# Kernel optimization log

Hardware: AMD Instinct MI355X
Metric: run time of the kernel (lower is better)

The kernel has to match this reference:

```python
import jax, jax.numpy as jnp
import numpy as np

NUM_HEADS = 16


def setup_inputs() -> dict:
    key = jax.random.key(0)
    k1, k2, k3, k4 = jax.random.split(key, 4)
    B, N, C = 4, 1024, 1024
    x = jax.random.normal(k1, (B, N, C), dtype=jnp.float32)
    mask = jnp.ones((B, N), dtype=jnp.float32)  # 1 = visible token
    # 0.02 init scale keeps logits in a sane range (avoids saturated softmax)
    W_qkv = jax.random.normal(k2, (C, 3 * C), dtype=jnp.float32) * 0.02
    W_proj = jax.random.normal(k3, (C, C), dtype=jnp.float32) * 0.02
    b_proj = jax.random.normal(k4, (C,), dtype=jnp.float32) * 0.02
    return {"x": x, "mask": mask, "W_qkv": W_qkv, "W_proj": W_proj, "b_proj": b_proj}


def reference(x, mask, W_qkv, W_proj, b_proj):
    B, N, C = x.shape
    H = NUM_HEADS
    D = C // H
    scale = D ** -0.5
    qkv = (x @ W_qkv).reshape(B, N, 3, H, D)
    q, k, v = qkv[:, :, 0], qkv[:, :, 1], qkv[:, :, 2]  # each [B, N, H, D]
    attn = jnp.einsum("bnhd,bmhd->bhnm", q, k) * scale  # [B, H, N, N]
    attn = attn + (1.0 - mask)[:, None, None, :] * -5.0  # additive mask penalty
    attn = jax.nn.softmax(attn, axis=-1)
    out = jnp.einsum("bhnm,bmhd->bnhd", attn, v).reshape(B, N, C)
    return out @ W_proj + b_proj
```

## Files before the change

kernel.cpp:

```cpp
#include <hip/hip_runtime.h>

typedef __attribute__((ext_vector_type(8))) short bf16x8;
typedef __attribute__((ext_vector_type(4))) float f32x4;
typedef __attribute__((ext_vector_type(16))) float f32x16;
typedef __attribute__((ext_vector_type(4))) float fl4;
typedef __attribute__((ext_vector_type(8))) unsigned short u16x8;
typedef __attribute__((ext_vector_type(4))) unsigned short u16x4;
typedef __attribute__((ext_vector_type(2))) int i32x2;
typedef __attribute__((ext_vector_type(4))) int i32x4;

#define MFMA16(A,B,C) __builtin_amdgcn_mfma_f32_16x16x32_bf16((A),(B),(C),0,0,0)
#define MFMA32(A,B,C) __builtin_amdgcn_mfma_f32_32x32x16_bf16((A),(B),(C),0,0,0)

__device__ __forceinline__ unsigned short f2bf_bits(float x) {
  union { float f; unsigned u; } v; v.f = x;
  unsigned r = v.u + 0x7fffu + ((v.u >> 16) & 1u);
  return (unsigned short)(r >> 16);
}

__device__ __forceinline__ void gload_lds16(const void* g, void* l) {
  __builtin_amdgcn_global_load_lds((const __attribute__((address_space(1))) void*)g,
                                   (__attribute__((address_space(3))) void*)l, 16, 0, 0);
}

__device__ __forceinline__ bf16x8 lds_frag(const char* base, int row, int bir) {
  int off = (row << 7) + bir;
  off ^= (row & 7) << 4;
  return *(const bf16x8*)(base + off);
}

__device__ __forceinline__ int cvtpk_bf16(float a, float b) {
  int r; asm("v_cvt_pk_bf16_f32 %0, %1, %2" : "=v"(r) : "v"(a), "v"(b)); return r;
}

__device__ __forceinline__ void plswap(int& a, int& b) {
#if __has_builtin(__builtin_amdgcn_permlane32_swap)
  i32x2 r = __builtin_amdgcn_permlane32_swap(a, b, false, false);
  a = r[0]; b = r[1];
#else
  asm volatile("s_nop 1\n\tv_permlane32_swap_b32 %0, %1" : "+v"(a), "+v"(b));
#endif
}

__global__ __launch_bounds__(256) void k_cvt(const float* __restrict__ src,
                                             unsigned short* __restrict__ dst, int n) {
  int i = (blockIdx.x * 256 + threadIdx.x) * 8;
  if (i >= n) return;
  fl4 a = *(const fl4*)(src + i);
  fl4 b = *(const fl4*)(src + i + 4);
  u16x8 o;
  o[0] = f2bf_bits(a[0]); o[1] = f2bf_bits(a[1]); o[2] = f2bf_bits(a[2]); o[3] = f2bf_bits(a[3]);
  o[4] = f2bf_bits(b[0]); o[5] = f2bf_bits(b[1]); o[6] = f2bf_bits(b[2]); o[7] = f2bf_bits(b[3]);
  *(u16x8*)(dst + i) = o;
}

__global__ __launch_bounds__(256) void k_tcvt(const float* __restrict__ src,
                                              unsigned short* __restrict__ dst, int NCOL) {
  __shared__ float tile[64][65];
  const int kt = blockIdx.y * 64, nt = blockIdx.x * 64;
  const int t = threadIdx.x;
  {
    int r = t >> 2, c0 = (t & 3) * 16;
    const float* s = src + (size_t)(kt + r) * NCOL + nt + c0;
    #pragma unroll
    for (int j = 0; j < 4; ++j) {
      fl4 v = *(const fl4*)(s + j * 4);
      tile[r][c0 + j * 4 + 0] = v[0]; tile[r][c0 + j * 4 + 1] = v[1];
      tile[r][c0 + j * 4 + 2] = v[2]; tile[r][c0 + j * 4 + 3] = v[3];
    }
  }
  __syncthreads();
  {
    int n = t >> 2, kc = (t & 3) * 16;
    unsigned short* d = dst + (size_t)(nt + n) * 1024 + kt + kc;
    u16x8 o0, o1;
    #pragma unroll
    for (int j = 0; j < 8; ++j) o0[j] = f2bf_bits(tile[kc + j][n]);
    #pragma unroll
    for (int j = 0; j < 8; ++j) o1[j] = f2bf_bits(tile[kc + 8 + j][n]);
    *(u16x8*)d = o0;
    *(u16x8*)(d + 8) = o1;
  }
}

template <int MODE>
__global__ __launch_bounds__(256) void k_gemm(const unsigned short* __restrict__ A,
                                              const unsigned short* __restrict__ Bt,
                                              unsigned short* __restrict__ qp,
                                              unsigned short* __restrict__ kp,
                                              unsigned short* __restrict__ vtp,
                                              const float* __restrict__ bias,
                                              float* __restrict__ outp) {
  __shared__ char lA[16384], lB[16384];
  const int tid = threadIdx.x, lane = tid & 63, w = tid >> 6;
  const int wm = w >> 1, wn = w & 1;
  const int m0 = blockIdx.y * 128, n0 = blockIdx.x * 128;
  const char* Ab = (const char*)A + (size_t)m0 * 2048;
  const char* Bb = (const char*)Bt + (size_t)n0 * 2048;

  f32x4 acc[4][4];
  #pragma unroll
  for (int mi = 0; mi < 4; ++mi)
    #pragma unroll
    for (int ni = 0; ni < 4; ++ni) acc[mi][ni] = f32x4{0.f, 0.f, 0.f, 0.f};

  for (int kt = 0; kt < 16; ++kt) {
    #pragma unroll
    for (int i = 0; i < 4; ++i) {
      int c = i * 256 + tid;
      int row = c >> 3, cc = c & 7, ccs = cc ^ (row & 7);
      char* dstA = lA + (i * 256 + w * 64) * 16;
      char* dstB = lB + (i * 256 + w * 64) * 16;
      gload_lds16(Ab + (size_t)row * 2048 + kt * 128 + ccs * 16, dstA);
      gload_lds16(Bb + (size_t)row * 2048 + kt * 128 + ccs * 16, dstB);
    }
    __syncthreads();
    #pragma unroll
    for (int ks = 0; ks < 2; ++ks) {
      bf16x8 af[4], bfv[4];
      #pragma unroll
      for (int mi = 0; mi < 4; ++mi)
        af[mi] = lds_frag(lA, wm * 64 + mi * 16 + (lane & 15), ks * 64 + ((lane >> 4) << 4));
      #pragma unroll
      for (int ni = 0; ni < 4; ++ni)
        bfv[ni] = lds_frag(lB, wn * 64 + ni * 16 + (lane & 15), ks * 64 + ((lane >> 4) << 4));
      #pragma unroll
      for (int mi = 0; mi < 4; ++mi)
        #pragma unroll
        for (int ni = 0; ni < 4; ++ni)
          acc[mi][ni] = MFMA16(af[mi], bfv[ni], acc[mi][ni]);
    }
    __syncthreads();
  }

  if (MODE == 0) {
    #pragma unroll
    for (int mi = 0; mi < 4; ++mi) {
      int row0 = m0 + wm * 64 + mi * 16 + ((lane >> 4) << 2);
      int bb = row0 >> 10, nn0 = row0 & 1023;
      #pragma unroll
      for (int ni = 0; ni < 4; ++ni) {
        int col = n0 + wn * 64 + ni * 16 + (lane & 15);
        int tt = col >> 10, rem = col & 1023, h = rem >> 6, d = rem & 63;
        f32x4 a = acc[mi][ni];
        if (tt == 2) {
          u16x4 pv;
          pv[0] = f2bf_bits(a[0]); pv[1] = f2bf_bits(a[1]);
          pv[2] = f2bf_bits(a[2]); pv[3] = f2bf_bits(a[3]);
          *(u16x4*)(vtp + (((size_t)(bb * 16 + h) * 64 + d) << 10) + nn0) = pv;
        } else {
          unsigned short* dst = (tt == 0) ? qp : kp;
          size_t base = ((size_t)(bb * 16 + h)) << 16;
          #pragma unroll
          for (int r = 0; r < 4; ++r)
            dst[base + (size_t)(nn0 + r) * 64 + d] = f2bf_bits(a[r]);
        }
      }
    }
  } else {
    #pragma unroll
    for (int mi = 0; mi < 4; ++mi) {
      int row0 = m0 + wm * 64 + mi * 16 + ((lane >> 4) << 2);
      #pragma unroll
      for (int ni = 0; ni < 4; ++ni) {
        int col = n0 + wn * 64 + ni * 16 + (lane & 15);
        float bv = bias[col];
        f32x4 a = acc[mi][ni];
        #pragma unroll
        for (int r = 0; r < 4; ++r)
          outp[(size_t)(row0 + r) * 1024 + col] = a[r] + bv;
      }
    }
  }
}

__global__ __launch_bounds__(256, 4) void k_attn(const unsigned short* __restrict__ qp,
                                                 const unsigned short* __restrict__ kp,
                                                 const unsigned short* __restrict__ vtp,
                                                 const float* __restrict__ mask,
                                                 unsigned short* __restrict__ aop) {
  __shared__ __align__(16) char lds[32768];
  const int tid = threadIdx.x, lane = tid & 63, w = tid >> 6;
  const int hi = lane >> 5, lq = lane & 31;
  const int pair = w >> 1;
  const int g = blockIdx.x;
  const int bh = (g & 7) * 8 + (g >> 7);
  const int qc = (g >> 3) & 15;
  const int b = bh >> 4, h = bh & 15;
  const char* kb = (const char*)(kp + ((size_t)bh << 16));
  const char* vb = (const char*)(vtp + ((size_t)bh << 16));
  const unsigned short* qh = qp + ((size_t)bh << 16);
  const float* mrow = mask + b * 1024 + pair * 512;
  const int q0 = qc * 64 + (w & 1) * 32;

  const int krow = tid >> 3, kslot = tid & 7;
  const int kcc = kslot ^ (krow & 7);
  const char* gKA = kb + (size_t)krow * 128 + kcc * 16;
  const char* gKB = gKA + 512 * 128;
  const int vrow = tid >> 2, vslot = tid & 3;
  const int vcc = vslot ^ ((vrow >> 1) & 3);
  const char* gVA = vb + (size_t)vrow * 2048 + vcc * 16;
  const char* gVB = gVA + 512 * 2;
  char* const dK = lds + tid * 16;
  char* const dV = lds + 8192 + tid * 16;

  const char* const myK = lds + pair * 4096;
  const char* const myV = lds + 8192 + pair * 4096;
  int kfo[4], vfo[4];
  #pragma unroll
  for (int dc = 0; dc < 4; ++dc)
    kfo[dc] = lq * 128 + (((dc << 1) | hi) ^ (lq & 7)) * 16;
  #pragma unroll
  for (int ks = 0; ks < 2; ++ks)
    #pragma unroll
    for (int nb = 0; nb < 2; ++nb) {
      int row = nb * 32 + lq;
      vfo[ks * 2 + nb] = row * 64 + (((ks << 1) | hi) ^ ((row >> 1) & 3)) * 16;
    }

  bf16x8 qB[4];
  #pragma unroll
  for (int dc = 0; dc < 4; ++dc)
    qB[dc] = *(const bf16x8*)(qh + (q0 + lq) * 64 + dc * 16 + hi * 8);

  i32x4 onesw = {hi == 0 ? 0x3F80 : 0, 0, 0, 0};
  const bf16x8 onesB = __builtin_bit_cast(bf16x8, onesw);

  f32x16 O0, O1;
  #pragma unroll
  for (int i = 0; i < 16; ++i) { O0[i] = 0.f; O1[i] = 0.f; }
  float lsum = 0.f;

#define STAGE(BUF, T)                                                          \
  do {                                                                         \
    gload_lds16(gKA + (T) * 4096, dK + (BUF) * 16384);                         \
    gload_lds16(gKB + (T) * 4096, dK + (BUF) * 16384 + 4096);                  \
    gload_lds16(gVA + (T) * 64,   dV + (BUF) * 16384);                         \
    gload_lds16(gVB + (T) * 64,   dV + (BUF) * 16384 + 4096);                  \
  } while (0)

#define STEP(BUF, T, LAST)                                                     \
  do {                                                                         \
    float mv = mrow[(T) * 32 + lq];                                            \
    if (!(LAST)) STAGE((BUF) ^ 1, (T) + 1);                                    \
    const char* K = myK + (BUF) * 16384;                                       \
    const char* V = myV + (BUF) * 16384;                                       \
    f32x16 acc;                                                                \
    _Pragma("unroll") for (int i = 0; i < 16; ++i) acc[i] = 0.f;               \
    __builtin_amdgcn_s_setprio(1);                                             \
    _Pragma("unroll") for (int dc = 0; dc < 4; ++dc) {                         \
      bf16x8 kf = *(const bf16x8*)(K + kfo[dc]);                               \
      acc = MFMA32(kf, qB[dc], acc);                                           \
    }                                                                          \
    __builtin_amdgcn_s_setprio(0);                                             \
    {                                                                          \
      int bw = (hi == 0) ? (int)f2bf_bits((1.0f - mv) * -40.0f) : 0;           \
      i32x4 bwv = {bw, 0, 0, 0};                                               \
      acc = MFMA32(__builtin_bit_cast(bf16x8, bwv), onesB, acc);               \
    }                                                                          \
    float p[16];                                                               \
    _Pragma("unroll") for (int r = 0; r < 16; ++r) {                           \
      p[r] = exp2f(fmaf(acc[r], 0.18033688f, -5.7707802f));                    \
      lsum += p[r];                                                            \
    }                                                                          \
    int X0 = cvtpk_bf16(p[0], p[1]),   X1 = cvtpk_bf16(p[2], p[3]);            \
    int Y0 = cvtpk_bf16(p[4], p[5]),   Y1 = cvtpk_bf16(p[6], p[7]);            \
    int Z0 = cvtpk_bf16(p[8], p[9]),   Z1 = cvtpk_bf16(p[10], p[11]);          \
    int V0 = cvtpk_bf16(p[12], p[13]), V1 = cvtpk_bf16(p[14], p[15]);          \
    plswap(X0, Y0); plswap(X1, Y1);                                            \
    plswap(Z0, V0); plswap(Z1, V1);                                            \
    i32x4 pa0v = {X0, X1, Y0, Y1};                                             \
    i32x4 pa1v = {Z0, Z1, V0, V1};                                             \
    const bf16x8 PA0 = __builtin_bit_cast(bf16x8, pa0v);                       \
    const bf16x8 PA1 = __builtin_bit_cast(bf16x8, pa1v);                       \
    bf16x8 va0 = *(const bf16x8*)(V + vfo[0]);                                 \
    bf16x8 va1 = *(const bf16x8*)(V + vfo[1]);                                 \
    bf16x8 vb0 = *(const bf16x8*)(V + vfo[2]);                                 \
    bf16x8 vb1 = *(const bf16x8*)(V + vfo[3]);                                 \
    __builtin_amdgcn_s_setprio(1);                                             \
    O0 = MFMA32(PA0, va0, O0);                                                 \
    O1 = MFMA32(PA0, va1, O1);                                                 \
    O0 = MFMA32(PA1, vb0, O0);                                                 \
    O1 = MFMA32(PA1, vb1, O1);                                                 \
    __builtin_amdgcn_s_setprio(0);                                             \
    __syncthreads();                                                           \
  } while (0)

  STAGE(0, 0);
  __syncthreads();
  for (int tt = 0; tt < 8; ++tt) {
    STEP(0, 2 * tt, 0);
    STEP(1, 2 * tt + 1, tt == 7);
  }
#undef STEP
#undef STAGE

  float tot = lsum + __shfl_xor(lsum, 32);
  float* fx = (float*)lds;
  if (pair == 1) {
    int base = (w - 2) * 64 * 34 + lane * 34;
    #pragma unroll
    for (int r = 0; r < 16; ++r) { fx[base + r] = O0[r]; fx[base + 16 + r] = O1[r]; }
    fx[base + 32] = tot;
  }
  __syncthreads();
  if (pair == 0) {
    int base = w * 64 * 34 + lane * 34;
    float invT = 1.0f / (tot + fx[base + 32]);
    #pragma unroll
    for (int r = 0; r < 16; ++r) {
      int qr = (r & 3) + 8 * (r >> 2) + 4 * hi;
      float iv = __shfl(invT, qr);
      float o0 = (O0[r] + fx[base + r]) * iv;
      float o1 = (O1[r] + fx[base + 16 + r]) * iv;
      size_t ob = (size_t)(b * 1024 + q0 + qr) * 1024 + h * 64 + lq;
      aop[ob] = f2bf_bits(o0);
      aop[ob + 32] = f2bf_bits(o1);
    }
  }
}

extern "C" void kernel_launch(void* const* d_in, const int* in_sizes, int n_in,
                              void* d_out, int out_size, void* d_ws, size_t ws_size,
                              hipStream_t stream) {
  const float* x     = (const float*)d_in[0];
  const float* mask  = (const float*)d_in[1];
  const float* wqkv  = (const float*)d_in[2];
  const float* wproj = (const float*)d_in[3];
  const float* bproj = (const float*)d_in[4];
  float* out = (float*)d_out;

  char* ws = (char*)d_ws;
  unsigned short* xb     = (unsigned short*)(ws);
  unsigned short* wqkvt  = (unsigned short*)(ws + 8388608);
  unsigned short* wprojt = (unsigned short*)(ws + 14680064);
  unsigned short* qbuf   = (unsigned short*)(ws + 16777216);
  unsigned short* kbuf   = (unsigned short*)(ws + 25165824);
  unsigned short* vtbuf  = (unsigned short*)(ws + 33554432);
  unsigned short* aobuf  = (unsigned short*)(ws + 41943040);

  k_cvt<<<dim3(2048), dim3(256), 0, stream>>>(x, xb, 4194304);
  k_tcvt<<<dim3(48, 16), dim3(256), 0, stream>>>(wqkv, wqkvt, 3072);
  k_tcvt<<<dim3(16, 16), dim3(256), 0, stream>>>(wproj, wprojt, 1024);
  k_gemm<0><<<dim3(24, 32), dim3(256), 0, stream>>>(xb, wqkvt, qbuf, kbuf, vtbuf, nullptr, nullptr);
  k_attn<<<dim3(1024), dim3(256), 0, stream>>>(qbuf, kbuf, vtbuf, mask, aobuf);
  k_gemm<1><<<dim3(8, 32), dim3(256), 0, stream>>>(aobuf, wprojt, nullptr, nullptr, nullptr, bproj, out);
}
```

Before: 106.3 us.

## Precompute mask bias in convert kernel and fold it into the exp argument

A per-token additive bias (mask penalty combined with the fixed softmax offset, in log2 units) is computed by extra blocks of the conversion kernel. The attention kernel adds this bias inside the exp2 FMA instead of issuing an extra MFMA per tile to inject the mask, and splits the row sum into two accumulators. The two weight-transpose launches are also merged into one to save a launch. This costs vector mask loads per step and a small workspace buffer.

```diff
diff --git a/kernel.cpp b/kernel.cpp
--- a/kernel.cpp
+++ b/kernel.cpp
@@ -43,8 +43,16 @@
 }
 
 __global__ __launch_bounds__(256) void k_cvt(const float* __restrict__ src,
-                                             unsigned short* __restrict__ dst, int n) {
-  int i = (blockIdx.x * 256 + threadIdx.x) * 8;
+                                             unsigned short* __restrict__ dst, int n,
+                                             const float* __restrict__ m,
+                                             float* __restrict__ mb) {
+  int bid = blockIdx.x;
+  if (bid >= 2048) {
+    int i = (bid - 2048) * 256 + threadIdx.x;
+    mb[i] = fmaf(m[i], 7.2134752f, -12.9842554f);
+    return;
+  }
+  int i = (bid * 256 + threadIdx.x) * 8;
   if (i >= n) return;
   fl4 a = *(const fl4*)(src + i);
   fl4 b = *(const fl4*)(src + i + 4);
@@ -54,10 +62,16 @@
   *(u16x8*)(dst + i) = o;
 }
 
-__global__ __launch_bounds__(256) void k_tcvt(const float* __restrict__ src,
-                                              unsigned short* __restrict__ dst, int NCOL) {
+__global__ __launch_bounds__(256) void k_tcvt2(const float* __restrict__ wqkv,
+                                               unsigned short* __restrict__ dqkv,
+                                               const float* __restrict__ wproj,
+                                               unsigned short* __restrict__ dproj) {
   __shared__ float tile[64][65];
-  const int kt = blockIdx.y * 64, nt = blockIdx.x * 64;
+  const int bx = blockIdx.x;
+  const float* src; unsigned short* dst; int NCOL, nt;
+  if (bx < 48) { src = wqkv; dst = dqkv; NCOL = 3072; nt = bx * 64; }
+  else         { src = wproj; dst = dproj; NCOL = 1024; nt = (bx - 48) * 64; }
+  const int kt = blockIdx.y * 64;
   const int t = threadIdx.x;
   {
     int r = t >> 2, c0 = (t & 3) * 16;
@@ -177,7 +191,7 @@
 __global__ __launch_bounds__(256, 4) void k_attn(const unsigned short* __restrict__ qp,
                                                  const unsigned short* __restrict__ kp,
                                                  const unsigned short* __restrict__ vtp,
-                                                 const float* __restrict__ mask,
+                                                 const float* __restrict__ mbias,
                                                  unsigned short* __restrict__ aop) {
   __shared__ __align__(16) char lds[32768];
   const int tid = threadIdx.x, lane = tid & 63, w = tid >> 6;
@@ -190,7 +204,7 @@
   const char* kb = (const char*)(kp + ((size_t)bh << 16));
   const char* vb = (const char*)(vtp + ((size_t)bh << 16));
   const unsigned short* qh = qp + ((size_t)bh << 16);
-  const float* mrow = mask + b * 1024 + pair * 512;
+  const float* mrow = mbias + b * 1024 + pair * 512;
   const int q0 = qc * 64 + (w & 1) * 32;
 
   const int krow = tid >> 3, kslot = tid & 7;
@@ -223,13 +237,10 @@
   for (int dc = 0; dc < 4; ++dc)
     qB[dc] = *(const bf16x8*)(qh + (q0 + lq) * 64 + dc * 16 + hi * 8);
 
-  i32x4 onesw = {hi == 0 ? 0x3F80 : 0, 0, 0, 0};
-  const bf16x8 onesB = __builtin_bit_cast(bf16x8, onesw);
-
   f32x16 O0, O1;
   #pragma unroll
   for (int i = 0; i < 16; ++i) { O0[i] = 0.f; O1[i] = 0.f; }
-  float lsum = 0.f;
+  float lsA = 0.f, lsB = 0.f;
 
 #define STAGE(BUF, T)                                                          \
   do {                                                                         \
@@ -241,7 +252,9 @@
 
 #define STEP(BUF, T, LAST)                                                     \
   do {                                                                         \
-    float mv = mrow[(T) * 32 + lq];                                            \
+    fl4 mw[4];                                                                 \
+    _Pragma("unroll") for (int g4 = 0; g4 < 4; ++g4)                           \
+      mw[g4] = *(const fl4*)(mrow + (T) * 32 + g4 * 8 + hi * 4);               \
     if (!(LAST)) STAGE((BUF) ^ 1, (T) + 1);                                    \
     const char* K = myK + (BUF) * 16384;                                       \
     const char* V = myV + (BUF) * 16384;                                       \
@@ -253,24 +266,19 @@
       acc = MFMA32(kf, qB[dc], acc);                                           \
     }                                                                          \
     __builtin_amdgcn_s_setprio(0);                                             \
-    {                                                                          \
-      int bw = (hi == 0) ? (int)f2bf_bits((1.0f - mv) * -40.0f) : 0;           \
-      i32x4 bwv = {bw, 0, 0, 0};                                               \
-      acc = MFMA32(__builtin_bit_cast(bf16x8, bwv), onesB, acc);               \
-    }                                                                          \
     float p[16];                                                               \
     _Pragma("unroll") for (int r = 0; r < 16; ++r) {                           \
-      p[r] = exp2f(fmaf(acc[r], 0.18033688f, -5.7707802f));                    \
-      lsum += p[r];                                                            \
+      p[r] = exp2f(fmaf(acc[r], 0.18033688f, mw[r >> 2][r & 3]));              \
+      if (r & 1) lsB += p[r]; else lsA += p[r];                                \
     }                                                                          \
     int X0 = cvtpk_bf16(p[0], p[1]),   X1 = cvtpk_bf16(p[2], p[3]);            \
     int Y0 = cvtpk_bf16(p[4], p[5]),   Y1 = cvtpk_bf16(p[6], p[7]);            \
     int Z0 = cvtpk_bf16(p[8], p[9]),   Z1 = cvtpk_bf16(p[10], p[11]);          \
-    int V0 = cvtpk_bf16(p[12], p[13]), V1 = cvtpk_bf16(p[14], p[15]);          \
+    int W0 = cvtpk_bf16(p[12], p[13]), W1 = cvtpk_bf16(p[14], p[15]);          \
     plswap(X0, Y0); plswap(X1, Y1);                                            \
-    plswap(Z0, V0); plswap(Z1, V1);                                            \
+    plswap(Z0, W0); plswap(Z1, W1);                                            \
     i32x4 pa0v = {X0, X1, Y0, Y1};                                             \
-    i32x4 pa1v = {Z0, Z1, V0, V1};                                             \
+    i32x4 pa1v = {Z0, Z1, W0, W1};                                             \
     const bf16x8 PA0 = __builtin_bit_cast(bf16x8, pa0v);                       \
     const bf16x8 PA1 = __builtin_bit_cast(bf16x8, pa1v);                       \
     bf16x8 va0 = *(const bf16x8*)(V + vfo[0]);                                 \
@@ -295,6 +303,7 @@
 #undef STEP
 #undef STAGE
 
+  float lsum = lsA + lsB;
   float tot = lsum + __shfl_xor(lsum, 32);
   float* fx = (float*)lds;
   if (pair == 1) {
@@ -338,11 +347,11 @@
   unsigned short* kbuf   = (unsigned short*)(ws + 25165824);
   unsigned short* vtbuf  = (unsigned short*)(ws + 33554432);
   unsigned short* aobuf  = (unsigned short*)(ws + 41943040);
-
-  k_cvt<<<dim3(2048), dim3(256), 0, stream>>>(x, xb, 4194304);
-  k_tcvt<<<dim3(48, 16), dim3(256), 0, stream>>>(wqkv, wqkvt, 3072);
-  k_tcvt<<<dim3(16, 16), dim3(256), 0, stream>>>(wproj, wprojt, 1024);
+  float*          mbias  = (float*)(ws + 50331648);
+
+  k_cvt<<<dim3(2064), dim3(256), 0, stream>>>(x, xb, 4194304, mask, mbias);
+  k_tcvt2<<<dim3(64, 16), dim3(256), 0, stream>>>(wqkv, wqkvt, wproj, wprojt);
   k_gemm<0><<<dim3(24, 32), dim3(256), 0, stream>>>(xb, wqkvt, qbuf, kbuf, vtbuf, nullptr, nullptr);
-  k_attn<<<dim3(1024), dim3(256), 0, stream>>>(qbuf, kbuf, vtbuf, mask, aobuf);
+  k_attn<<<dim3(1024), dim3(256), 0, stream>>>(qbuf, kbuf, vtbuf, mbias, aobuf);
   k_gemm<1><<<dim3(8, 32), dim3(256), 0, stream>>>(aobuf, wprojt, nullptr, nullptr, nullptr, bproj, out);
 }
```

Result: slower. 109.8 us (+3.3%).
